# Performance work log

Measured on AMD Instinct MI355X. Metric: run time of the kernel, lower is better.

## Reference

```python
import jax, jax.numpy as jnp
import numpy as np


def setup_inputs() -> dict:
    key = jax.random.key(0)
    kx, kq, kk, kv = jax.random.split(key, 4)
    d_model, d_head = 1024, 64
    x = jax.random.normal(kx, (4, 4096, d_model), dtype=jnp.float32)
    scale = 1.0 / np.sqrt(d_model)
    Wq = jax.random.normal(kq, (d_model, d_head), dtype=jnp.float32) * scale
    Wk = jax.random.normal(kk, (d_model, d_head), dtype=jnp.float32) * scale
    Wv = jax.random.normal(kv, (d_model, d_head), dtype=jnp.float32) * scale
    return {"x": x, "Wq": Wq, "Wk": Wk, "Wv": Wv}


def reference(x, Wq, Wk, Wv):
    # x: [B, S, D]; Wq/Wk/Wv: [D, H]
    d_head = Wq.shape[-1]
    Q = jnp.einsum('bsd,dh->bsh', x, Wq)
    K = jnp.einsum('bsd,dh->bsh', x, Wk)
    V = jnp.einsum('bsd,dh->bsh', x, Wv)
    scores = jnp.einsum('bqh,bkh->bqk', Q, K) / jnp.sqrt(jnp.float32(d_head))
    S = x.shape[1]
    causal = jnp.tril(jnp.ones((S, S), dtype=bool))  # [S, S]
    scores = jnp.where(causal, scores, -jnp.inf)
    weights = jax.nn.softmax(scores, axis=-1)  # [B, S, S]
    return jnp.einsum('bqk,bkh->bqh', weights, V)
```

## Files before the change

kernel.cpp:

```cpp
#include <hip/hip_runtime.h>

#define D_MODEL 1024
#define D_HEAD  64
#define SEQ     4096
#define BATCH   4
#define M_TOT   (BATCH * SEQ)
#define LOG2E   1.44269504088896f
#define MFIX_L2 17.3123404906676f
#define CHUNK   16

typedef __bf16 bf16;
typedef bf16  bf16x8 __attribute__((ext_vector_type(8)));
typedef bf16  bf16x4v __attribute__((ext_vector_type(4)));
typedef float f32x4  __attribute__((ext_vector_type(4)));

#define MFMA(a, b, c) __builtin_amdgcn_mfma_f32_16x16x32_bf16(a, b, c, 0, 0, 0)

__device__ __forceinline__ void phase_barrier() {
    __builtin_amdgcn_sched_barrier(0);
    asm volatile("s_waitcnt vmcnt(0)" ::: "memory");
    __builtin_amdgcn_s_barrier();
    __builtin_amdgcn_sched_barrier(0);
}

__device__ __forceinline__ void gld16(const void* g, void* l) {
    __builtin_amdgcn_global_load_lds(
        (const __attribute__((address_space(1))) void*)g,
        (__attribute__((address_space(3))) void*)l, 16, 0, 0);
}

#define QKV_OFF  0
#define OBUF_OFF 6291456
#define LBUF_OFF 10485760
#define WT_OFF   10551296
#define VT_OFF   10944512

__global__ void prep_kernel(const float* __restrict__ Wq, const float* __restrict__ Wk,
                            const float* __restrict__ Wv, bf16* __restrict__ Wt,
                            float4* __restrict__ zp, int n4)
{
    const int bx = blockIdx.x;
    const int t  = threadIdx.x;
    if (bx < 48) {
        __shared__ bf16 tr[64][72];
        const int wm = bx >> 4, kt = bx & 15, k0 = kt * 64;
        const float* W = (wm == 0) ? Wq : (wm == 1) ? Wk : Wv;
        const int kr = t >> 2, nb = (t & 3) * 16;
        #pragma unroll
        for (int j = 0; j < 4; j++) {
            float4 wrow = *(const float4*)(W + (size_t)(k0 + kr) * D_HEAD + nb + j * 4);
            tr[nb + j * 4 + 0][kr] = (bf16)wrow.x;
            tr[nb + j * 4 + 1][kr] = (bf16)wrow.y;
            tr[nb + j * 4 + 2][kr] = (bf16)wrow.z;
            tr[nb + j * 4 + 3][kr] = (bf16)wrow.w;
        }
        __syncthreads();
        const int n = t >> 2, kc = (t & 3) * 8;
        bf16* dst = Wt + (size_t)(wm * 64 + n) * D_MODEL + k0;
        #pragma unroll
        for (int h = 0; h < 2; h++) {
            bf16x8 v;
            #pragma unroll
            for (int j = 0; j < 8; j++) v[j] = tr[n][kc + h * 32 + j];
            *(bf16x8*)(dst + kc + h * 32) = v;
        }
    } else {
        int i = (bx - 48) * 256 + t;
        if (i < n4) zp[i] = float4{0.f, 0.f, 0.f, 0.f};
    }
}

__global__ __launch_bounds__(256, 2) void proj_kernel(
    const float* __restrict__ x, const bf16* __restrict__ Wt,
    bf16* __restrict__ qkv, bf16* __restrict__ vt)
{
    __shared__ __align__(16) char Al[2][32 * 256];
    __shared__ __align__(16) char Bl[2][192 * 128];

    const int t    = threadIdx.x;
    const int wv   = t >> 6;
    const int lane = t & 63;
    const int quad = lane >> 4;
    const int l15  = lane & 15;
    const int row0 = blockIdx.x * 32;

    const char* xb = (const char*)x;
    const char* wb = (const char*)Wt;

    f32x4 acc[6] = {};

    auto stageA = [&](int bsel, int step) {
        #pragma unroll
        for (int i = 0; i < 2; i++) {
            const int s  = wv * 2 + i;
            const int r  = s * 4 + (lane >> 4);
            const int cs = ((lane & 15) * 16) ^ ((r & 7) << 4);
            const void* g = xb + (size_t)(row0 + r) * 4096 + step * 256 + cs;
            gld16(g, (char*)Al[bsel] + s * 1024);
        }
    };
    auto stageB = [&](int bsel, int step) {
        #pragma unroll
        for (int i = 0; i < 6; i++) {
            const int s  = wv * 6 + i;
            const int n  = s * 8 + (lane >> 3);
            const int cs = ((lane & 7) * 16) ^ ((n & 7) << 4);
            const void* g = wb + (size_t)n * 2048 + step * 128 + cs;
            gld16(g, (char*)Bl[bsel] + s * 1024);
        }
    };

    auto cvt8 = [](float4 lo, float4 hi) {
        bf16x8 r;
        r[0] = (bf16)lo.x; r[1] = (bf16)lo.y; r[2] = (bf16)lo.z; r[3] = (bf16)lo.w;
        r[4] = (bf16)hi.x; r[5] = (bf16)hi.y; r[6] = (bf16)hi.z; r[7] = (bf16)hi.w;
        return r;
    };

    auto compute = [&](int bsel) {
        const char* Ab = Al[bsel];
        const char* Bb = Bl[bsel];
        #pragma unroll
        for (int ks = 0; ks < 2; ks++) {
            bf16x8 afr[2];
            #pragma unroll
            for (int rg = 0; rg < 2; rg++) {
                const int r  = rg * 16 + l15;
                const int o  = ks * 128 + quad * 32;
                const int m  = (r & 7) << 4;
                float4 lo = *(const float4*)(Ab + r * 256 + (o ^ m));
                float4 hi = *(const float4*)(Ab + r * 256 + ((o + 16) ^ m));
                afr[rg] = cvt8(lo, hi);
            }
            #pragma unroll
            for (int j = 0; j < 3; j++) {
                const int n  = wv * 48 + j * 16 + l15;
                const int o  = ks * 64 + quad * 16;
                bf16x8 bfrg = *(const bf16x8*)(Bb + n * 128 + (o ^ ((n & 7) << 4)));
                acc[0 * 3 + j] = MFMA(afr[0], bfrg, acc[0 * 3 + j]);
                acc[1 * 3 + j] = MFMA(afr[1], bfrg, acc[1 * 3 + j]);
            }
        }
    };

    stageA(0, 0);
    stageB(0, 0);
    phase_barrier();

    int buf = 0;
    for (int s = 0; s < 16; s++) {
        if (s + 1 < 16) {
            stageA(buf ^ 1, s + 1);
            stageB(buf ^ 1, s + 1);
        }
        compute(buf);
        phase_barrier();
        buf ^= 1;
    }

    const int bb = row0 >> 12, s0 = row0 & (SEQ - 1);
    #pragma unroll
    for (int rg = 0; rg < 2; rg++)
        #pragma unroll
        for (int j = 0; j < 3; j++) {
            const int col = wv * 48 + j * 16 + l15;
            const int wm = col >> 6, h = col & 63;
            if (wm == 2) {
                bf16x4v vv;
                #pragma unroll
                for (int r = 0; r < 4; r++)
                    vv[r] = (bf16)acc[rg * 3 + j][r];
                *(bf16x4v*)(vt + ((size_t)bb * D_HEAD + h) * SEQ +
                            s0 + rg * 16 + quad * 4) = vv;
            } else {
                const float sc = (wm == 0) ? 0.125f : 1.0f;
                bf16* outp = qkv + (size_t)wm * M_TOT * D_HEAD;
                #pragma unroll
                for (int r = 0; r < 4; r++) {
                    const int row = row0 + rg * 16 + quad * 4 + r;
                    outp[(size_t)row * D_HEAD + h] =
                        (bf16)(acc[rg * 3 + j][r] * sc);
                }
            }
        }
}

__global__ __launch_bounds__(256, 4) void attn_kernel(
    const bf16* __restrict__ qkv, const bf16* __restrict__ vt,
    float* __restrict__ o_buf, float* __restrict__ l_buf)
{
    const int i = blockIdx.x;
    const int c = blockIdx.y;
    const int b = blockIdx.z;
    const int ntiles = i + 1;
    const int tile0  = c * CHUNK;
    if (tile0 >= ntiles) return;
    const int tile1 = min(tile0 + CHUNK, ntiles);

    __shared__ __align__(16) char KsB[2 * 64 * 128];
    __shared__ __align__(16) char VsB[2 * 64 * 128];

    auto kaddr = [](char* base, int pp, int row, int colb) -> void* {
        return base + pp * 8192 + row * 128 + (colb ^ ((row & 7) << 4));
    };

    const bf16* Q = qkv;
    const bf16* K = qkv + (size_t)M_TOT * D_HEAD;

    const int t    = threadIdx.x;
    const int wv   = t >> 6;
    const int lane = t & 63;
    const int quad = lane >> 4;
    const int l15  = lane & 15;
    const int qb   = i * 64;
    const size_t base  = (size_t)b * SEQ * D_HEAD;
    const bf16* vtb = vt + (size_t)b * D_HEAD * SEQ;

    bf16x8 qf0, qf1;
    {
        const bf16* qr = Q + base + (size_t)(qb + wv * 16 + l15) * D_HEAD;
        qf0 = *(const bf16x8*)(qr + quad * 8);
        qf1 = *(const bf16x8*)(qr + 32 + quad * 8);
    }

    f32x4 o[4] = {};
    float lsum = 0.f;
    const int qw0 = qb + wv * 16;

    const char* Kb = (const char*)(K + base);
    const char* Vb = (const char*)vtb;

    auto stage_kv = [&](int tile, int pp) {
        #pragma unroll
        for (int i2 = 0; i2 < 2; i2++) {
            const int s  = wv * 2 + i2;
            const int rr = s * 8 + (lane >> 3);
            const int sw = ((lane & 7) * 16) ^ ((lane >> 3) << 4);
            gld16(Kb + (size_t)(tile * 64 + rr) * 128 + sw,
                  KsB + pp * 8192 + s * 1024);
            gld16(Vb + (size_t)rr * (SEQ * 2) + (size_t)tile * 128 + sw,
                  VsB + pp * 8192 + s * 1024);
        }
    };

    stage_kv(tile0, 0);
    phase_barrier();

    int p = 0;
    for (int tile = tile0; tile < tile1; tile++) {
        const int kk0 = tile * 64;

        if (tile + 1 < tile1) stage_kv(tile + 1, p ^ 1);

        f32x4 sc4[4];
        __builtin_amdgcn_s_setprio(1);
        #pragma unroll
        for (int kt = 0; kt < 4; kt++) {
            f32x4 z = {};
            z = MFMA(*(bf16x8*)kaddr(KsB, p, kt * 16 + l15, quad * 16),      qf0, z);
            z = MFMA(*(bf16x8*)kaddr(KsB, p, kt * 16 + l15, 64 + quad * 16), qf1, z);
            sc4[kt] = z;
        }
        __builtin_amdgcn_s_setprio(0);

        bf16 ph[4][4];
        if (tile == i) {
            #pragma unroll
            for (int kt = 0; kt < 4; kt++)
                #pragma unroll
                for (int r = 0; r < 4; r++) {
                    float s = sc4[kt][r];
                    if (kk0 + kt * 16 + quad * 4 + r > qw0 + l15)
                        s = -1e30f;
                    float pe = __builtin_amdgcn_exp2f(fmaf(s, LOG2E, -MFIX_L2));
                    lsum += pe;
                    ph[kt][r] = (bf16)pe;
                }
        } else {
            #pragma unroll
            for (int kt = 0; kt < 4; kt++)
                #pragma unroll
                for (int r = 0; r < 4; r++) {
                    float pe = __builtin_amdgcn_exp2f(
                        fmaf(sc4[kt][r], LOG2E, -MFIX_L2));
                    lsum += pe;
                    ph[kt][r] = (bf16)pe;
                }
        }

        unsigned pku[4][2];
        #pragma unroll
        for (int kt = 0; kt < 4; kt++) {
            __builtin_memcpy(&pku[kt][0], &ph[kt][0], 4);
            __builtin_memcpy(&pku[kt][1], &ph[kt][2], 4);
        }

        const int srcA = l15 + ((lane & 16) ? 32 : 0);
        const int srcB = srcA + 16;
        const bool hi  = (lane & 32) != 0;

        #pragma unroll
        for (int c2 = 0; c2 < 2; c2++) {
            unsigned xA0 = __shfl((int)pku[2 * c2][0],     srcA);
            unsigned xA1 = __shfl((int)pku[2 * c2][1],     srcA);
            unsigned yA0 = __shfl((int)pku[2 * c2 + 1][0], srcA);
            unsigned yA1 = __shfl((int)pku[2 * c2 + 1][1], srcA);
            unsigned xB0 = __shfl((int)pku[2 * c2][0],     srcB);
            unsigned xB1 = __shfl((int)pku[2 * c2][1],     srcB);
            unsigned yB0 = __shfl((int)pku[2 * c2 + 1][0], srcB);
            unsigned yB1 = __shfl((int)pku[2 * c2 + 1][1], srcB);
            unsigned fr[4];
            fr[0] = hi ? yA0 : xA0;
            fr[1] = hi ? yA1 : xA1;
            fr[2] = hi ? yB0 : xB0;
            fr[3] = hi ? yB1 : xB1;
            bf16x8 pa;
            __builtin_memcpy(&pa, fr, 16);

            __builtin_amdgcn_s_setprio(1);
            #pragma unroll
            for (int t4 = 0; t4 < 4; t4++) {
                bf16x8 vb = *(bf16x8*)kaddr(VsB, p, t4 * 16 + l15,
                                            c2 * 64 + quad * 16);
                o[t4] = MFMA(pa, vb, o[t4]);
            }
            __builtin_amdgcn_s_setprio(0);
        }

        if (tile + 1 < tile1) phase_barrier();
        p ^= 1;
    }

    const int mrow0 = b * SEQ + qw0;
    lsum += __shfl_xor(lsum, 16, 64);
    lsum += __shfl_xor(lsum, 32, 64);
    if (lane < 16)
        atomicAdd(&l_buf[mrow0 + l15], lsum);
    #pragma unroll
    for (int r = 0; r < 4; r++) {
        const size_t orow = (size_t)(mrow0 + quad * 4 + r) * D_HEAD;
        #pragma unroll
        for (int t4 = 0; t4 < 4; t4++)
            atomicAdd(&o_buf[orow + t4 * 16 + l15], o[t4][r]);
    }
}

__global__ void norm_kernel(const float4* __restrict__ o_buf,
                            const float* __restrict__ l_buf,
                            float4* __restrict__ out)
{
    int gid = blockIdx.x * 256 + threadIdx.x;
    int m = gid >> 4;
    float inv = 1.0f / l_buf[m];
    float4 v = o_buf[gid];
    out[gid] = float4{v.x * inv, v.y * inv, v.z * inv, v.w * inv};
}

extern "C" void kernel_launch(void* const* d_in, const int* in_sizes, int n_in,
                              void* d_out, int out_size, void* d_ws, size_t ws_size,
                              hipStream_t stream) {
    const float* x  = (const float*)d_in[0];
    const float* Wq = (const float*)d_in[1];
    const float* Wk = (const float*)d_in[2];
    const float* Wv = (const float*)d_in[3];

    bf16*  qkv   = (bf16*)((char*)d_ws + QKV_OFF);
    float* o_buf = (float*)((char*)d_ws + OBUF_OFF);
    float* l_buf = (float*)((char*)d_ws + LBUF_OFF);
    bf16*  Wt    = (bf16*)((char*)d_ws + WT_OFF);
    bf16*  vt    = (bf16*)((char*)d_ws + VT_OFF);

    const int zero4 = (M_TOT * 65) / 4;
    const int zblocks = (zero4 + 255) / 256;
    prep_kernel<<<48 + zblocks, 256, 0, stream>>>(Wq, Wk, Wv, Wt,
                                                  (float4*)o_buf, zero4);
    proj_kernel<<<M_TOT / 32, 256, 0, stream>>>(x, Wt, qkv, vt);
    attn_kernel<<<dim3(SEQ / 64, SEQ / 64 / CHUNK, BATCH), 256, 0, stream>>>(
        qkv, vt, o_buf, l_buf);
    norm_kernel<<<M_TOT * 16 / 256, 256, 0, stream>>>((const float4*)o_buf, l_buf,
                                                      (float4*)d_out);
}
```

Measured before the change: 150.9 us.

## Triple-buffer loads in projection and attention kernels, enlarge projection tile

Both the projection and attention kernels move from double to triple buffering of LDS tiles. Each iteration now waits with a partial vmcnt, keeping one prefetch in flight, and uses a single barrier per iteration instead of two. The projection kernel also grows to 512 threads covering 64 rows per block, so B-matrix (weight) tiles are reused across two row groups. The cost is more LDS per block, which lowers occupancy: attention launch bounds drop from 4 to 3 blocks and projection runs one block per CU.

```diff
diff --git a/kernel.cpp b/kernel.cpp
--- a/kernel.cpp
+++ b/kernel.cpp
@@ -16,12 +16,12 @@
 
 #define MFMA(a, b, c) __builtin_amdgcn_mfma_f32_16x16x32_bf16(a, b, c, 0, 0, 0)
 
-__device__ __forceinline__ void phase_barrier() {
-    __builtin_amdgcn_sched_barrier(0);
-    asm volatile("s_waitcnt vmcnt(0)" ::: "memory");
-    __builtin_amdgcn_s_barrier();
-    __builtin_amdgcn_sched_barrier(0);
-}
+#define WAIT_BARRIER(N) do {                                       \
+    __builtin_amdgcn_sched_barrier(0);                             \
+    asm volatile("s_waitcnt vmcnt(" #N ")" ::: "memory");          \
+    __builtin_amdgcn_s_barrier();                                  \
+    __builtin_amdgcn_sched_barrier(0);                             \
+} while (0)
 
 __device__ __forceinline__ void gld16(const void* g, void* l) {
     __builtin_amdgcn_global_load_lds(
@@ -70,19 +70,21 @@
     }
 }
 
-__global__ __launch_bounds__(256, 2) void proj_kernel(
+__global__ __launch_bounds__(512, 1) void proj_kernel(
     const float* __restrict__ x, const bf16* __restrict__ Wt,
     bf16* __restrict__ qkv, bf16* __restrict__ vt)
 {
-    __shared__ __align__(16) char Al[2][32 * 256];
-    __shared__ __align__(16) char Bl[2][192 * 128];
+    __shared__ __align__(16) char Al[3][64 * 256];
+    __shared__ __align__(16) char Bl[3][192 * 128];
 
     const int t    = threadIdx.x;
-    const int wv   = t >> 6;
+    const int w    = t >> 6;
+    const int rg2  = w >> 2;
+    const int nw   = w & 3;
     const int lane = t & 63;
     const int quad = lane >> 4;
     const int l15  = lane & 15;
-    const int row0 = blockIdx.x * 32;
+    const int row0 = blockIdx.x * 64;
 
     const char* xb = (const char*)x;
     const char* wb = (const char*)Wt;
@@ -92,21 +94,21 @@
     auto stageA = [&](int bsel, int step) {
         #pragma unroll
         for (int i = 0; i < 2; i++) {
-            const int s  = wv * 2 + i;
+            const int s  = w * 2 + i;
             const int r  = s * 4 + (lane >> 4);
             const int cs = ((lane & 15) * 16) ^ ((r & 7) << 4);
-            const void* g = xb + (size_t)(row0 + r) * 4096 + step * 256 + cs;
-            gld16(g, (char*)Al[bsel] + s * 1024);
+            gld16(xb + (size_t)(row0 + r) * 4096 + step * 256 + cs,
+                  (char*)Al[bsel] + s * 1024);
         }
     };
     auto stageB = [&](int bsel, int step) {
         #pragma unroll
-        for (int i = 0; i < 6; i++) {
-            const int s  = wv * 6 + i;
+        for (int i = 0; i < 3; i++) {
+            const int s  = w * 3 + i;
             const int n  = s * 8 + (lane >> 3);
             const int cs = ((lane & 7) * 16) ^ ((n & 7) << 4);
-            const void* g = wb + (size_t)n * 2048 + step * 128 + cs;
-            gld16(g, (char*)Bl[bsel] + s * 1024);
+            gld16(wb + (size_t)n * 2048 + step * 128 + cs,
+                  (char*)Bl[bsel] + s * 1024);
         }
     };
 
@@ -125,7 +127,7 @@
             bf16x8 afr[2];
             #pragma unroll
             for (int rg = 0; rg < 2; rg++) {
-                const int r  = rg * 16 + l15;
+                const int r  = rg2 * 32 + rg * 16 + l15;
                 const int o  = ks * 128 + quad * 32;
                 const int m  = (r & 7) << 4;
                 float4 lo = *(const float4*)(Ab + r * 256 + (o ^ m));
@@ -134,36 +136,37 @@
             }
             #pragma unroll
             for (int j = 0; j < 3; j++) {
-                const int n  = wv * 48 + j * 16 + l15;
+                const int n  = nw * 48 + j * 16 + l15;
                 const int o  = ks * 64 + quad * 16;
                 bf16x8 bfrg = *(const bf16x8*)(Bb + n * 128 + (o ^ ((n & 7) << 4)));
-                acc[0 * 3 + j] = MFMA(afr[0], bfrg, acc[0 * 3 + j]);
-                acc[1 * 3 + j] = MFMA(afr[1], bfrg, acc[1 * 3 + j]);
+                acc[j]     = MFMA(afr[0], bfrg, acc[j]);
+                acc[3 + j] = MFMA(afr[1], bfrg, acc[3 + j]);
             }
         }
     };
 
-    stageA(0, 0);
-    stageB(0, 0);
-    phase_barrier();
+    stageA(0, 0); stageB(0, 0);
+    stageA(1, 1); stageB(1, 1);
 
     int buf = 0;
     for (int s = 0; s < 16; s++) {
-        if (s + 1 < 16) {
-            stageA(buf ^ 1, s + 1);
-            stageB(buf ^ 1, s + 1);
+        if (s + 1 < 16) { WAIT_BARRIER(5); }
+        else            { WAIT_BARRIER(0); }
+        if (s + 2 < 16) {
+            int nb2 = buf + 2; if (nb2 >= 3) nb2 -= 3;
+            stageA(nb2, s + 2); stageB(nb2, s + 2);
         }
         compute(buf);
-        phase_barrier();
-        buf ^= 1;
-    }
-
-    const int bb = row0 >> 12, s0 = row0 & (SEQ - 1);
+        buf = (buf == 2) ? 0 : buf + 1;
+    }
+
+    const int bb = row0 >> 12, s0v = row0 & (SEQ - 1);
+    const int rbase = rg2 * 32;
     #pragma unroll
     for (int rg = 0; rg < 2; rg++)
         #pragma unroll
         for (int j = 0; j < 3; j++) {
-            const int col = wv * 48 + j * 16 + l15;
+            const int col = nw * 48 + j * 16 + l15;
             const int wm = col >> 6, h = col & 63;
             if (wm == 2) {
                 bf16x4v vv;
@@ -171,13 +174,13 @@
                 for (int r = 0; r < 4; r++)
                     vv[r] = (bf16)acc[rg * 3 + j][r];
                 *(bf16x4v*)(vt + ((size_t)bb * D_HEAD + h) * SEQ +
-                            s0 + rg * 16 + quad * 4) = vv;
+                            s0v + rbase + rg * 16 + quad * 4) = vv;
             } else {
                 const float sc = (wm == 0) ? 0.125f : 1.0f;
                 bf16* outp = qkv + (size_t)wm * M_TOT * D_HEAD;
                 #pragma unroll
                 for (int r = 0; r < 4; r++) {
-                    const int row = row0 + rg * 16 + quad * 4 + r;
+                    const int row = row0 + rbase + rg * 16 + quad * 4 + r;
                     outp[(size_t)row * D_HEAD + h] =
                         (bf16)(acc[rg * 3 + j][r] * sc);
                 }
@@ -185,7 +188,7 @@
         }
 }
 
-__global__ __launch_bounds__(256, 4) void attn_kernel(
+__global__ __launch_bounds__(256, 3) void attn_kernel(
     const bf16* __restrict__ qkv, const bf16* __restrict__ vt,
     float* __restrict__ o_buf, float* __restrict__ l_buf)
 {
@@ -197,8 +200,8 @@
     if (tile0 >= ntiles) return;
     const int tile1 = min(tile0 + CHUNK, ntiles);
 
-    __shared__ __align__(16) char KsB[2 * 64 * 128];
-    __shared__ __align__(16) char VsB[2 * 64 * 128];
+    __shared__ __align__(16) char KsB[3 * 64 * 128];
+    __shared__ __align__(16) char VsB[3 * 64 * 128];
 
     auto kaddr = [](char* base, int pp, int row, int colb) -> void* {
         return base + pp * 8192 + row * 128 + (colb ^ ((row & 7) << 4));
@@ -244,13 +247,19 @@
     };
 
     stage_kv(tile0, 0);
-    phase_barrier();
+    if (tile0 + 1 < tile1) stage_kv(tile0 + 1, 1);
 
     int p = 0;
     for (int tile = tile0; tile < tile1; tile++) {
         const int kk0 = tile * 64;
 
-        if (tile + 1 < tile1) stage_kv(tile + 1, p ^ 1);
+        if (tile + 1 < tile1) { WAIT_BARRIER(4); }
+        else                  { WAIT_BARRIER(0); }
+
+        if (tile + 2 < tile1) {
+            int nb2 = p + 2; if (nb2 >= 3) nb2 -= 3;
+            stage_kv(tile + 2, nb2);
+        }
 
         f32x4 sc4[4];
         __builtin_amdgcn_s_setprio(1);
@@ -327,8 +336,7 @@
             __builtin_amdgcn_s_setprio(0);
         }
 
-        if (tile + 1 < tile1) phase_barrier();
-        p ^= 1;
+        p = (p == 2) ? 0 : p + 1;
     }
 
     const int mrow0 = b * SEQ + qw0;
@@ -374,7 +382,7 @@
     const int zblocks = (zero4 + 255) / 256;
     prep_kernel<<<48 + zblocks, 256, 0, stream>>>(Wq, Wk, Wv, Wt,
                                                   (float4*)o_buf, zero4);
-    proj_kernel<<<M_TOT / 32, 256, 0, stream>>>(x, Wt, qkv, vt);
+    proj_kernel<<<M_TOT / 64, 512, 0, stream>>>(x, Wt, qkv, vt);
     attn_kernel<<<dim3(SEQ / 64, SEQ / 64 / CHUNK, BATCH), 256, 0, stream>>>(
         qkv, vt, o_buf, l_buf);
     norm_kernel<<<M_TOT * 16 / 256, 256, 0, stream>>>((const float4*)o_buf, l_buf,
```

New measurement: 149.7 us. Within noise of the previous version (-0.8%).
